# Kernel optimization log

Hardware: AMD Instinct MI355X
Metric: run time of the kernel (lower is better)

Reference implementation:

```python
import jax, jax.numpy as jnp
import numpy as np
import math

H = 256; LAT = 128; T = 1024; B = 64
FREQS = jnp.array([0.19, 0.21, 0.23, 0.25, 0.27, 0.29], dtype=jnp.float32)
EPS = 1e-5  # torch LayerNorm / BatchNorm default eps


def layer_norm(x, g, b):
    m = x.mean(-1, keepdims=True)
    v = jnp.var(x, axis=-1, keepdims=True)
    return (x - m) / jnp.sqrt(v + EPS) * g + b


def lrelu(x):
    return jax.nn.leaky_relu(x, 0.2)


def lstm_layer(x, wih, whh, bih, bhh):
    # x: [B,T,I] -> outputs [B,T,Hh]; PyTorch gate order i,f,g,o
    Hh = whh.shape[1]
    xg = jnp.einsum('bti,gi->btg', x, wih) + bih + bhh  # precomputed input contribution
    def step(carry, xg_t):
        h, c = carry
        gates = xg_t + h @ whh.T
        i, f, g, o = jnp.split(gates, 4, axis=-1)
        c = jax.nn.sigmoid(f) * c + jax.nn.sigmoid(i) * jnp.tanh(g)
        h = jax.nn.sigmoid(o) * jnp.tanh(c)
        return (h, c), h
    h0 = jnp.zeros((x.shape[0], Hh), x.dtype)
    _, hs = jax.lax.scan(step, (h0, h0), jnp.swapaxes(xg, 0, 1))
    return jnp.swapaxes(hs, 0, 1)


def conv1d(x, w, b, pad):
    # x [B,C,T], w [O,I,K]
    y = jax.lax.conv_general_dilated(x, w, (1,), [(pad, pad)],
                                     dimension_numbers=('NCH', 'OIH', 'NCH'))
    return y + b[None, :, None]


def bn_eval(x, g, b):
    # eval-mode BatchNorm1d with running_mean=0, running_var=1
    return x / jnp.sqrt(1.0 + EPS) * g[None, :, None] + b[None, :, None]


def setup_inputs() -> dict:
    key = jax.random.key(0)
    ks = iter(jax.random.split(key, 64))
    def w(shape, s=0.05):
        return (s * jax.random.normal(next(ks), shape)).astype(jnp.float32)
    z1 = jnp.zeros
    o1 = jnp.ones
    inp = dict(
        z=jax.random.normal(next(ks), (B, LAT), dtype=jnp.float32),
        labels=jax.random.randint(next(ks), (B,), 0, 4),
        emb=w((4, H)),
        np_w=w((H, LAT + H)), np_b=z1((H,)), np_ln_g=o1((H,)), np_ln_b=z1((H,)),
        c_wih=w((4 * H, 2 * H)), c_whh=w((4 * H, H)), c_bih=z1((4 * H,)), c_bhh=z1((4 * H,)),
        f0_wih=w((4 * H, 2 * H)), f0_whh=w((4 * H, H)), f0_bih=z1((4 * H,)), f0_bhh=z1((4 * H,)),
        f_wih=w((3, 4 * H, H)), f_whh=w((3, 4 * H, H)), f_bih=z1((3, 4 * H)), f_bhh=z1((3, 4 * H)),
        osc_w1=w((H, H)), osc_b1=z1((H,)), osc_ln_g=o1((H,)), osc_ln_b=z1((H,)),
        osc_w2=w((T, H)), osc_b2=z1((T,)),
        cp_w1=w((H // 2, 2 * H)), cp_b1=z1((H // 2,)), cp_ln_g=o1((H // 2,)), cp_ln_b=z1((H // 2,)),
        cp_w2=w((4, H // 2)), cp_b2=z1((4,)),
        sin_w=w((H // 2, 12)), sin_b=z1((H // 2,)),
        conv1_w=w((H, 2 * H, 5)), conv1_b=z1((H,)), bn1_g=o1((H,)), bn1_b=z1((H,)),
        conv2_w=w((H // 2, H, 3)), conv2_b=z1((H // 2,)), bn2_g=o1((H // 2,)), bn2_b=z1((H // 2,)),
        conv3_w=w((1, H // 2, 3)), conv3_b=z1((1,)),
        stress_w=jnp.full((1, 1, 1), 1.8, dtype=jnp.float32),
        amuse_w=jnp.array([[[0.15, 0.7, 0.15]]], dtype=jnp.float32),
        amuse_b=jnp.full((1,), -0.3, dtype=jnp.float32),
    )
    return inp


def reference(z, labels, emb, np_w, np_b, np_ln_g, np_ln_b,
              c_wih, c_whh, c_bih, c_bhh,
              f0_wih, f0_whh, f0_bih, f0_bhh,
              f_wih, f_whh, f_bih, f_bhh,
              osc_w1, osc_b1, osc_ln_g, osc_ln_b, osc_w2, osc_b2,
              cp_w1, cp_b1, cp_ln_g, cp_ln_b, cp_w2, cp_b2,
              sin_w, sin_b,
              conv1_w, conv1_b, bn1_g, bn1_b,
              conv2_w, conv2_b, bn2_g, bn2_b,
              conv3_w, conv3_b, stress_w, amuse_w, amuse_b):
    Bn = z.shape[0]
    le = emb[labels]                                                    # [B,H]
    h = lrelu(layer_norm(jnp.concatenate([z, le], -1) @ np_w.T + np_b, np_ln_g, np_ln_b))
    sig_in = jnp.concatenate([jnp.broadcast_to(h[:, None, :], (Bn, T, H)),
                              jnp.broadcast_to(le[:, None, :], (Bn, T, H))], -1)  # [B,T,2H]
    coarse = lstm_layer(sig_in, c_wih, c_whh, c_bih, c_bhh)
    fine = lstm_layer(sig_in, f0_wih, f0_whh, f0_bih, f0_bhh)
    for l in range(f_wih.shape[0]):
        fine = lstm_layer(fine, f_wih[l], f_whh[l], f_bih[l], f_bhh[l])
    osc = jnp.tanh(lrelu(layer_norm(h @ osc_w1.T + osc_b1, osc_ln_g, osc_ln_b)) @ osc_w2.T + osc_b2)[:, :, None]  # [B,T,1]
    t = jnp.linspace(0.0, 1.0, T)
    phases = 2.0 * math.pi * t[:, None] * FREQS[None, :] * T            # [T,6]
    sincos = jnp.concatenate([jnp.sin(phases), jnp.cos(phases)], -1)    # [T,12]
    sin_feat = sincos @ sin_w.T + sin_b                                 # [T,H/2]
    sin_mean = jnp.broadcast_to(sin_feat.mean(-1, keepdims=True)[None], (Bn, T, 1))
    feats = jnp.concatenate([coarse.mean(1), fine.mean(1)], -1)         # [B,2H] (vectorized per-sample loop)
    cp = jax.nn.sigmoid(lrelu(layer_norm(feats @ cp_w1.T + cp_b1, cp_ln_g, cp_ln_b)) @ cp_w2.T + cp_b2)  # [B,4]
    freq = 0.19 + 0.1 * cp[:, 0:1]
    amp = 1.0 + 2.0 * cp[:, 1:2]
    phase = 2.0 * math.pi * cp[:, 2:3]
    baseline = -0.5 + cp[:, 3:4]
    cardiac = (amp * jnp.sin(2.0 * math.pi * freq * T * t[None, :] + phase) + baseline)[:, :, None]  # [B,T,1]
    combined = jnp.swapaxes(jnp.concatenate([coarse, fine], -1), 1, 2)  # [B,2H,T]
    x = lrelu(bn_eval(conv1d(combined, conv1_w, conv1_b, 2), bn1_g, bn1_b))
    x = lrelu(bn_eval(conv1d(x, conv2_w, conv2_b, 1), bn2_g, bn2_b))
    base = jnp.swapaxes(jnp.tanh(conv1d(x, conv3_w, conv3_b, 1)), 1, 2)  # [B,T,1]
    enhanced = 0.1 * base + 0.1 * osc + 0.7 * cardiac + 0.1 * sin_mean
    # vectorized per-sample conditional routing (expert dispatch)
    et = jnp.swapaxes(enhanced, 1, 2)                                   # [B,1,T]
    stress = jnp.swapaxes(conv1d(et, stress_w, jnp.zeros((1,), et.dtype), 0), 1, 2)
    amuse = jnp.swapaxes(conv1d(et, amuse_w, amuse_b, 1), 1, 2)
    lab = labels[:, None, None]
    out = jnp.where(lab == 1, enhanced,
                    jnp.where(lab == 2, stress,
                              jnp.where(lab == 3, amuse, jnp.zeros_like(enhanced))))
    return out
```

## Files before the change

kernel.cpp:

```cpp
#include <hip/hip_runtime.h>

typedef _Float16 f16;
typedef _Float16 f16x2 __attribute__((ext_vector_type(2)));
typedef _Float16 f16x8 __attribute__((ext_vector_type(8)));
typedef float    f32x4 __attribute__((ext_vector_type(4)));

__device__ f16   g_Xpad [64u*1028u*512u];
__device__ f16   g_fseqA[64u*1024u*256u];
__device__ f16   g_fseqB[64u*1024u*256u];
__device__ f16   g_fseqC[64u*1024u*256u];
__device__ float g_xg32 [3u*64u*1048576u];
__device__ f16   g_c2in [64u*1026u*256u];
__device__ f16   g_c3in [64u*1024u*128u];
__device__ f16   g_whhT2[5u*262144u];
__device__ f16   g_wihO [3u*262144u];
__device__ float g_biasP[3*1024];
__device__ f16   g_B1   [256u*2560u];
__device__ f16   g_B2   [128u*768u];
__device__ float g_xg0  [2*64*1024];
__device__ float g_cat512[64*512];
__device__ float g_h    [64*256];
__device__ float g_feats[64*512];
__device__ float g_osc  [64*1024];
__device__ float g_smean[1024];
__device__ float g_cpar [64*4];
__device__ float g_enh  [64*1024];
__device__ unsigned g_hflag[3*64*128];
__device__ unsigned g_pflag[3*64*128];

__device__ inline float fdot2f(f16x2 a, f16x2 b, float c) {
#if __has_builtin(__builtin_amdgcn_fdot2)
  return __builtin_amdgcn_fdot2(a, b, c, false);
#else
  return c + (float)a[0]*(float)b[0] + (float)a[1]*(float)b[1];
#endif
}
__device__ inline float sigm_fast(float x) { return 1.0f / (1.0f + __expf(-x)); }
__device__ inline float tanh_fast(float x) { float e = __expf(2.0f*x); return 1.0f - 2.0f/(e + 1.0f); }
__device__ inline float lrelu(float x) { return x < 0.0f ? 0.2f*x : x; }
__device__ __forceinline__ void dot8x(f16x8 w, f16x8 h, float& a) {
  a = fdot2f(__builtin_shufflevector(w, w, 0, 1), __builtin_shufflevector(h, h, 0, 1), a);
  a = fdot2f(__builtin_shufflevector(w, w, 2, 3), __builtin_shufflevector(h, h, 2, 3), a);
  a = fdot2f(__builtin_shufflevector(w, w, 4, 5), __builtin_shufflevector(h, h, 4, 5), a);
  a = fdot2f(__builtin_shufflevector(w, w, 6, 7), __builtin_shufflevector(h, h, 6, 7), a);
}
__device__ __forceinline__ void wait_ge(const unsigned* p, unsigned want) {
  while (__hip_atomic_load(p, __ATOMIC_RELAXED, __HIP_MEMORY_SCOPE_AGENT) < want) {}
  unsigned v;
  do { v = __hip_atomic_load(p, __ATOMIC_ACQUIRE, __HIP_MEMORY_SCOPE_AGENT); } while (v < want);
}

__global__ void __launch_bounds__(256) k_prep_whh(const float* cw, const float* f0w, const float* fw) {
  int bid = blockIdx.x;
  int L = bid >> 10, g = bid & 1023, k = threadIdx.x;
  const float* src = (L == 0) ? cw : (L == 1) ? f0w : (fw + (size_t)(L-2)*262144u);
  int q = g >> 8, u = g & 255, r = u*4 + q;
  int ko = k >> 3, kl = k & 7;
  g_whhT2[(size_t)L*262144u + (size_t)(ko*1024 + r)*8u + kl] = (f16)src[(size_t)g*256 + k];
}
__global__ void __launch_bounds__(256) k_prep_wih(const float* fwih, const float* fbih, const float* fbhh) {
  int bid = blockIdx.x;
  int L = bid >> 10, g = bid & 1023, k = threadIdx.x;
  int q = g >> 8, u = g & 255, r = u*4 + q;
  int ko = k >> 3, kl = k & 7;
  g_wihO[(size_t)L*262144u + (size_t)(ko*1024 + r)*8u + kl] = (f16)fwih[(size_t)L*262144u + (size_t)g*256u + k];
  if (k == 0) g_biasP[L*1024 + r] = fbih[L*1024 + g] + fbhh[L*1024 + g];
}
__global__ void __launch_bounds__(256) k_prep_c1(const float* w) {
  int idx = blockIdx.x*256 + threadIdx.x;
  int oc = idx / 2560, rem = idx % 2560, r = rem / 512, ic = rem % 512;
  g_B1[idx] = (f16)w[(size_t)oc*2560 + (size_t)ic*5 + r];
}
__global__ void __launch_bounds__(256) k_prep_c2(const float* w) {
  int idx = blockIdx.x*256 + threadIdx.x;
  int oc = idx / 768, rem = idx % 768, r = rem / 256, ic = rem % 256;
  g_B2[idx] = (f16)w[(size_t)oc*768 + (size_t)ic*3 + r];
}
__global__ void __launch_bounds__(256) k_zero() {
  int idx = blockIdx.x*256 + threadIdx.x;
  if (idx < 131072) {
    int b = idx >> 11, rem = idx & 2047, rr = rem >> 9, c = rem & 511;
    int row = (rr < 2) ? rr : 1024 + rr;
    g_Xpad[(size_t)b*526336u + (size_t)row*512u + c] = (f16)0.0f;
  } else if (idx < 163840) {
    int i2 = idx - 131072;
    int b = i2 >> 9, rem = i2 & 511, rr = rem >> 8, c = rem & 255;
    int row = rr ? 1025 : 0;
    g_c2in[(size_t)b*262656u + (size_t)row*256u + c] = (f16)0.0f;
  } else {
    int i3 = idx - 163840;
    if (i3 < 24576) g_hflag[i3] = 0u;
    else            g_pflag[i3 - 24576] = 0u;
  }
}

__global__ void __launch_bounds__(256) k_setup1(const float* z, const int* labels, const float* emb,
                                                const float* npw, const float* npb,
                                                const float* lg, const float* lb) {
  __shared__ float x[384];
  __shared__ float s1[256], s2[256];
  int b = blockIdx.x, tid = threadIdx.x;
  int lab = labels[b];
  for (int i = tid; i < 384; i += 256)
    x[i] = (i < 128) ? z[b*128 + i] : emb[lab*256 + (i - 128)];
  __syncthreads();
  float acc = npb[tid];
  for (int k = 0; k < 384; ++k) acc += npw[tid*384 + k]*x[k];
  s1[tid] = acc; s2[tid] = acc*acc; __syncthreads();
  for (int s = 128; s > 0; s >>= 1) { if (tid < s) { s1[tid]+=s1[tid+s]; s2[tid]+=s2[tid+s]; } __syncthreads(); }
  float m = s1[0]*(1.0f/256.0f), var = s2[0]*(1.0f/256.0f) - m*m;
  float hv = (acc - m)*(1.0f/sqrtf(var + 1e-5f))*lg[tid] + lb[tid];
  hv = lrelu(hv);
  g_h[b*256 + tid] = hv;
  g_cat512[b*512 + tid] = hv;
  g_cat512[b*512 + 256 + tid] = x[128 + tid];
}
__global__ void __launch_bounds__(1024) k_xg0(const float* cwih, const float* cbih, const float* cbhh,
                                              const float* fwih, const float* fbih, const float* fbhh) {
  int bid = blockIdx.x;
  int layer = bid >> 6, b = bid & 63;
  int gp = threadIdx.x, j = gp >> 2, q = gp & 3, g = q*256 + j;
  __shared__ float cat[512];
  if (gp < 512) cat[gp] = g_cat512[b*512 + gp];
  __syncthreads();
  const float* w = layer ? fwih : cwih;
  float acc = layer ? (fbih[g] + fbhh[g]) : (cbih[g] + cbhh[g]);
  for (int k = 0; k < 512; ++k) acc += w[(size_t)g*512 + k]*cat[k];
  g_xg0[(layer*64 + b)*1024 + gp] = acc;
}
__global__ void __launch_bounds__(256) k_osc(const float* w1, const float* b1v, const float* lg,
                                             const float* lb, const float* w2, const float* b2v) {
  __shared__ float hb[256], av[256], s1[256], s2[256];
  int b = blockIdx.x, tid = threadIdx.x;
  hb[tid] = g_h[b*256 + tid];
  __syncthreads();
  float acc = b1v[tid];
  for (int k = 0; k < 256; ++k) acc += w1[tid*256 + k]*hb[k];
  s1[tid] = acc; s2[tid] = acc*acc; __syncthreads();
  for (int s = 128; s > 0; s >>= 1) { if (tid < s) { s1[tid]+=s1[tid+s]; s2[tid]+=s2[tid+s]; } __syncthreads(); }
  float m = s1[0]*(1.0f/256.0f), var = s2[0]*(1.0f/256.0f) - m*m;
  av[tid] = lrelu((acc - m)*(1.0f/sqrtf(var + 1e-5f))*lg[tid] + lb[tid]);
  __syncthreads();
  for (int tt = tid; tt < 1024; tt += 256) {
    float o = b2v[tt];
    for (int i = 0; i < 256; ++i) o += w2[(size_t)tt*256 + i]*av[i];
    g_osc[b*1024 + tt] = tanhf(o);
  }
}
__global__ void __launch_bounds__(256) k_sinmean(const float* sw, const float* sb) {
  int tt = blockIdx.x*256 + threadIdx.x;
  const float F[6] = {0.19f, 0.21f, 0.23f, 0.25f, 0.27f, 0.29f};
  float tl = tt*(1.0f/1023.0f);
  float sc[12];
  for (int j = 0; j < 6; ++j) {
    float p = (6.2831853071795864f * tl) * F[j] * 1024.0f;
    sc[j] = sinf(p); sc[6 + j] = cosf(p);
  }
  float a = 0.0f;
  for (int i = 0; i < 128; ++i) {
    float s = sb[i];
    for (int j = 0; j < 12; ++j) s += sw[i*12 + j]*sc[j];
    a += s;
  }
  g_smean[tt] = a*(1.0f/128.0f);
}

__global__ void __launch_bounds__(512, 2) k_chain() {
  int bid = blockIdx.x;
  int role = bid >> 6, b = bid & 63;
  int tau = threadIdx.x;
  bool isP = (role == 2) || (role == 4) || (role == 6);
  int lp = (role - 2) >> 1;
  int Lg = (role==0)?0:(role==1)?1:(role==3)?2:(role==5)?3:4;

  __shared__ __align__(16) f16 wlds[65536];
  __shared__ __align__(16) f16 hbuf[2][256];
  __shared__ __align__(16) float gbuf[1024];

  const f16* Wc = isP ? (g_wihO + (size_t)lp*262144u) : (g_whhT2 + (size_t)Lg*262144u);
#pragma unroll
  for (int i = 0; i < 16; ++i) {
    int o = i*512 + tau;
    *(f16x8*)(wlds + (size_t)o*8u) = *(const f16x8*)(Wc + (size_t)o*8u);
  }
  f16x8 wA[24], wB[24];
  {
    const f16* wp = Wc + (size_t)(8*1024 + tau)*8u;
#pragma unroll
    for (int i = 0; i < 24; ++i) {
      wA[i] = *(const f16x8*)(wp + (size_t)i*8192u);
      wB[i] = *(const f16x8*)(wp + (size_t)i*8192u + 4096u);
    }
  }

  if (isP) {
    const f16* hs = ((lp==0) ? g_fseqA : (lp==1) ? g_fseqB : g_fseqC) + (size_t)b*262144u;
    const unsigned* hf = g_hflag + (lp*64 + b)*128;
    float* xo = g_xg32 + (size_t)(lp*64 + b)*1048576u;
    unsigned* pf = g_pflag + (lp*64 + b)*128;
    float bA = g_biasP[lp*1024 + tau], bB = g_biasP[lp*1024 + 512 + tau];
    __syncthreads();
#pragma unroll 1
    for (int t = 0; t < 1024; ++t) {
      if ((t & 7) == 0) {
        if (tau == 0) wait_ge(hf + (t >> 3), (unsigned)(t >> 3) + 1u);
        __syncthreads();
      }
      if (tau < 32) *(f16x8*)(&hbuf[t & 1][tau*8]) = *(const f16x8*)(hs + (size_t)t*256u + tau*8);
      __syncthreads();
      const f16* hb = &hbuf[t & 1][0];
      float a0 = 0.f, a1 = 0.f, b0 = 0.f, b1 = 0.f;
#pragma unroll
      for (int ko = 0; ko < 8; ++ko) {
        f16x8 hv = *(const f16x8*)(hb + ko*8);
        f16x8 wa = *(const f16x8*)(wlds + (size_t)(ko*1024 + tau)*8u);
        f16x8 wb = *(const f16x8*)(wlds + (size_t)(ko*1024 + tau + 512)*8u);
        dot8x(wa, hv, a0); dot8x(wb, hv, b0);
      }
#pragma unroll
      for (int i = 0; i < 24; ++i) {
        f16x8 hv = *(const f16x8*)(hb + 64 + i*8);
        dot8x(wA[i], hv, a1); dot8x(wB[i], hv, b1);
      }
      xo[(size_t)t*1024u + tau]       = a0 + a1 + bA;
      xo[(size_t)t*1024u + 512 + tau] = b0 + b1 + bB;
      if ((t & 7) == 7) {
        __syncthreads();
        if (tau == 0) __hip_atomic_store(pf + (t >> 3), (unsigned)(t >> 3) + 1u,
                                         __ATOMIC_RELEASE, __HIP_MEMORY_SCOPE_AGENT);
      }
    }
  } else {
    bool dyn = (role >= 3);
    int lq = (role - 3) >> 1;
    float c0 = 0.0f, sum0 = 0.0f;
    f32x4 xg4 = {0.f, 0.f, 0.f, 0.f};
    const f32x4* xp = nullptr;
    const unsigned* xf = nullptr;
    f16* outp = nullptr; int ostride = 0;
    unsigned* hfo = nullptr;
    if (tau < 256) {
      hbuf[0][tau] = (f16)0.0f;
      if (!dyn) xg4 = *(const f32x4*)(g_xg0 + (size_t)(Lg*64 + b)*1024u + 4*tau);
      else      xp  = (const f32x4*)(g_xg32 + (size_t)(lq*64 + b)*1048576u) + tau;
      if (role == 0)      { outp = g_Xpad  + (size_t)b*526336u + 1024 + tau;       ostride = 512; }
      else if (role == 1) { outp = g_fseqA + (size_t)b*262144u + tau;              ostride = 256; }
      else if (role == 3) { outp = g_fseqB + (size_t)b*262144u + tau;              ostride = 256; }
      else if (role == 5) { outp = g_fseqC + (size_t)b*262144u + tau;              ostride = 256; }
      else                { outp = g_Xpad  + (size_t)b*526336u + 1024 + 256 + tau; ostride = 512; }
    }
    if (dyn) xf = g_pflag + (lq*64 + b)*128;
    int hop = (role == 1) ? 0 : (role == 3) ? 1 : (role == 5) ? 2 : -1;
    if (hop >= 0) hfo = g_hflag + (hop*64 + b)*128;
    __syncthreads();
    int cur = 0;
#pragma unroll 1
    for (int step = 0; step < 1024; ++step) {
      if (dyn && (step & 7) == 0) {
        if (tau == 0) wait_ge(xf + (step >> 3), (unsigned)(step >> 3) + 1u);
        __syncthreads();
      }
      f32x4 xv = xg4;
      if (dyn && tau < 256)
        xv = xp[(size_t)step*256u];
      const f16* hb = &hbuf[cur][0];
      float a0 = 0.f, a1 = 0.f, b0 = 0.f, b1 = 0.f;
#pragma unroll
      for (int ko = 0; ko < 8; ++ko) {
        f16x8 hv = *(const f16x8*)(hb + ko*8);
        f16x8 wa = *(const f16x8*)(wlds + (size_t)(ko*1024 + tau)*8u);
        f16x8 wb = *(const f16x8*)(wlds + (size_t)(ko*1024 + tau + 512)*8u);
        dot8x(wa, hv, a0); dot8x(wb, hv, b0);
      }
#pragma unroll
      for (int i = 0; i < 24; ++i) {
        f16x8 hv = *(const f16x8*)(hb + 64 + i*8);
        dot8x(wA[i], hv, a1); dot8x(wB[i], hv, b1);
      }
      gbuf[tau] = a0 + a1; gbuf[tau + 512] = b0 + b1;
      __syncthreads();
      if (tau < 256) {
        f32x4 gv = *(const f32x4*)(&gbuf[4*tau]);
        float ii = sigm_fast(gv[0] + xv[0]), ff = sigm_fast(gv[1] + xv[1]);
        float gg = tanh_fast(gv[2] + xv[2]), oo = sigm_fast(gv[3] + xv[3]);
        c0 = ff*c0 + ii*gg;
        float h0 = oo*tanh_fast(c0); sum0 += h0;
        hbuf[cur ^ 1][tau] = (f16)h0;
        outp[(size_t)step*ostride] = (f16)h0;
      }
      __syncthreads();
      if (hfo && (step & 7) == 7 && tau == 0)
        __hip_atomic_store(hfo + (step >> 3), (unsigned)(step >> 3) + 1u,
                           __ATOMIC_RELEASE, __HIP_MEMORY_SCOPE_AGENT);
      cur ^= 1;
    }
    if (tau < 256) {
      if (role == 0) g_feats[b*512 + tau]       = sum0*(1.0f/1024.0f);
      if (role == 7) g_feats[b*512 + 256 + tau] = sum0*(1.0f/1024.0f);
    }
  }
}

__global__ void __launch_bounds__(256) k_gemm(int which,
                                              const float* cb, const float* bng, const float* bnb) {
  const f16* A; size_t a_bs; int a_rs, K; const f16* Bm;
  f16* outH; size_t o_bs; int o_rs;
  if (which == 2) {
    A = g_Xpad; a_bs = 526336u; a_rs = 512; K = 2560; Bm = g_B1;
    outH = g_c2in + 256; o_bs = 262656u; o_rs = 256;
  } else {
    A = g_c2in; a_bs = 262656u; a_rs = 256; K = 768; Bm = g_B2;
    outH = g_c3in; o_bs = 131072u; o_rs = 128;
  }
  int tid = threadIdx.x, wave = tid >> 6, lane = tid & 63;
  int m0 = blockIdx.x*128, n0 = blockIdx.y*64;
  __shared__ __align__(16) f16 Asm[128*72];
  __shared__ __align__(16) f16 Bsm[64*72];
  f32x4 acc[2][4];
#pragma unroll
  for (int i = 0; i < 2; ++i)
#pragma unroll
    for (int jj = 0; jj < 4; ++jj) { f32x4 zz = {0.f,0.f,0.f,0.f}; acc[i][jj] = zz; }
  int ar = tid & 127, ac = (tid >> 7)*32;
  int mrow = m0 + ar, abb = mrow >> 10, att = mrow & 1023;
  const f16* aptr = A + (size_t)abb*a_bs + (size_t)att*a_rs + ac;
  int br = tid & 63, bc = (tid >> 6)*16;
  const f16* bptr = Bm + (size_t)(n0 + br)*K + bc;
  int nkb = K >> 6;
  for (int kb = 0; kb < nkb; ++kb) {
    f16x8 av0 = *(const f16x8*)(aptr + 0);
    f16x8 av1 = *(const f16x8*)(aptr + 8);
    f16x8 av2 = *(const f16x8*)(aptr + 16);
    f16x8 av3 = *(const f16x8*)(aptr + 24);
    f16x8 bv0 = *(const f16x8*)(bptr + 0);
    f16x8 bv1 = *(const f16x8*)(bptr + 8);
    aptr += 64; bptr += 64;
    __syncthreads();
    *(f16x8*)(&Asm[ar*72 + ac + 0])  = av0;
    *(f16x8*)(&Asm[ar*72 + ac + 8])  = av1;
    *(f16x8*)(&Asm[ar*72 + ac + 16]) = av2;
    *(f16x8*)(&Asm[ar*72 + ac + 24]) = av3;
    *(f16x8*)(&Bsm[br*72 + bc + 0])  = bv0;
    *(f16x8*)(&Bsm[br*72 + bc + 8])  = bv1;
    __syncthreads();
#pragma unroll
    for (int ks = 0; ks < 2; ++ks) {
      int ko = ks*32 + (lane >> 4)*8;
      f16x8 a0 = *(const f16x8*)(&Asm[(wave*32 + (lane & 15))*72 + ko]);
      f16x8 a1 = *(const f16x8*)(&Asm[(wave*32 + 16 + (lane & 15))*72 + ko]);
#pragma unroll
      for (int nt = 0; nt < 4; ++nt) {
        f16x8 bf = *(const f16x8*)(&Bsm[(nt*16 + (lane & 15))*72 + ko]);
        acc[0][nt] = __builtin_amdgcn_mfma_f32_16x16x32_f16(a0, bf, acc[0][nt], 0, 0, 0);
        acc[1][nt] = __builtin_amdgcn_mfma_f32_16x16x32_f16(a1, bf, acc[1][nt], 0, 0, 0);
      }
    }
  }
  const float bnc = 0.99999500003749969f;
#pragma unroll
  for (int mt = 0; mt < 2; ++mt)
#pragma unroll
    for (int nt = 0; nt < 4; ++nt)
#pragma unroll
      for (int r = 0; r < 4; ++r) {
        int m_loc = wave*32 + mt*16 + (lane >> 4)*4 + r;
        int n = n0 + nt*16 + (lane & 15);
        int mg = m0 + m_loc, ob = mg >> 10, ot = mg & 1023;
        float v = acc[mt][nt][r];
        v = (v + cb[n])*(bng[n]*bnc) + bnb[n];
        v = lrelu(v);
        outH[(size_t)ob*o_bs + (size_t)ot*o_rs + n] = (f16)v;
      }
}

__global__ void __launch_bounds__(128) k_cp(const float* w1, const float* b1v, const float* lg,
                                            const float* lb, const float* w2, const float* b2v) {
  __shared__ float ft[512], av[128], s1[128], s2[128];
  int b = blockIdx.x, tid = threadIdx.x;
  for (int i = tid; i < 512; i += 128) ft[i] = g_feats[b*512 + i];
  __syncthreads();
  float acc = b1v[tid];
  for (int k = 0; k < 512; ++k) acc += w1[tid*512 + k]*ft[k];
  s1[tid] = acc; s2[tid] = acc*acc; __syncthreads();
  for (int s = 64; s > 0; s >>= 1) { if (tid < s) { s1[tid]+=s1[tid+s]; s2[tid]+=s2[tid+s]; } __syncthreads(); }
  float m = s1[0]*(1.0f/128.0f), var = s2[0]*(1.0f/128.0f) - m*m;
  av[tid] = lrelu((acc - m)*(1.0f/sqrtf(var + 1e-5f))*lg[tid] + lb[tid]);
  __syncthreads();
  if (tid < 4) {
    float s = b2v[tid];
    for (int i = 0; i < 128; ++i) s += w2[tid*128 + i]*av[i];
    g_cpar[b*4 + tid] = 1.0f/(1.0f + expf(-s));
  }
}

__global__ void __launch_bounds__(256) k_enh(const float* w3, const float* b3) {
  int idx = blockIdx.x*256 + threadIdx.x;
  int b = idx >> 10, t = idx & 1023;
  const f16* xc = g_c3in + (size_t)idx*128u;
  bool hm = (t > 0), hp = (t < 1023);
  float pre = b3[0];
  for (int c = 0; c < 128; ++c) {
    float xm = hm ? (float)xc[c - 128] : 0.0f;
    float x0 = (float)xc[c];
    float xp = hp ? (float)xc[c + 128] : 0.0f;
    pre += xm*w3[c*3] + x0*w3[c*3 + 1] + xp*w3[c*3 + 2];
  }
  float base = tanhf(pre);
  float cp0 = g_cpar[b*4 + 0], cp1 = g_cpar[b*4 + 1], cp2 = g_cpar[b*4 + 2], cp3 = g_cpar[b*4 + 3];
  float freq  = 0.19f + 0.1f*cp0;
  float amp   = 1.0f + 2.0f*cp1;
  float phase = 6.2831853071795864f*cp2;
  float basel = -0.5f + cp3;
  float tl = t*(1.0f/1023.0f);
  float arg = ((6.2831853071795864f*freq)*1024.0f)*tl + phase;
  float card = amp*sinf(arg) + basel;
  g_enh[idx] = 0.1f*base + 0.1f*g_osc[idx] + 0.7f*card + 0.1f*g_smean[t];
}

__global__ void __launch_bounds__(256) k_out(const int* labels, const float* sw,
                                             const float* aw, const float* ab, float* out) {
  int idx = blockIdx.x*256 + threadIdx.x;
  int b = idx >> 10, t = idx & 1023;
  int lab = labels[b];
  float e = g_enh[idx], r;
  if (lab == 1) r = e;
  else if (lab == 2) r = sw[0]*e;
  else if (lab == 3) {
    float em = (t > 0)    ? g_enh[idx - 1] : 0.0f;
    float ep = (t < 1023) ? g_enh[idx + 1] : 0.0f;
    r = aw[0]*em + aw[1]*e + aw[2]*ep + ab[0];
  } else r = 0.0f;
  out[idx] = r;
}

extern "C" void kernel_launch(void* const* d_in, const int* in_sizes, int n_in,
                              void* d_out, int out_size, void* d_ws, size_t ws_size,
                              hipStream_t stream) {
  const float* z       = (const float*)d_in[0];
  const int*   labels  = (const int*)  d_in[1];
  const float* emb     = (const float*)d_in[2];
  const float* np_w    = (const float*)d_in[3];
  const float* np_b    = (const float*)d_in[4];
  const float* np_ln_g = (const float*)d_in[5];
  const float* np_ln_b = (const float*)d_in[6];
  const float* c_wih   = (const float*)d_in[7];
  const float* c_whh   = (const float*)d_in[8];
  const float* c_bih   = (const float*)d_in[9];
  const float* c_bhh   = (const float*)d_in[10];
  const float* f0_wih  = (const float*)d_in[11];
  const float* f0_whh  = (const float*)d_in[12];
  const float* f0_bih  = (const float*)d_in[13];
  const float* f0_bhh  = (const float*)d_in[14];
  const float* f_wih   = (const float*)d_in[15];
  const float* f_whh   = (const float*)d_in[16];
  const float* f_bih   = (const float*)d_in[17];
  const float* f_bhh   = (const float*)d_in[18];
  const float* osc_w1  = (const float*)d_in[19];
  const float* osc_b1  = (const float*)d_in[20];
  const float* osc_ln_g= (const float*)d_in[21];
  const float* osc_ln_b= (const float*)d_in[22];
  const float* osc_w2  = (const float*)d_in[23];
  const float* osc_b2  = (const float*)d_in[24];
  const float* cp_w1   = (const float*)d_in[25];
  const float* cp_b1   = (const float*)d_in[26];
  const float* cp_ln_g = (const float*)d_in[27];
  const float* cp_ln_b = (const float*)d_in[28];
  const float* cp_w2   = (const float*)d_in[29];
  const float* cp_b2   = (const float*)d_in[30];
  const float* sin_w   = (const float*)d_in[31];
  const float* sin_b   = (const float*)d_in[32];
  const float* conv1_w = (const float*)d_in[33];
  const float* conv1_b = (const float*)d_in[34];
  const float* bn1_g   = (const float*)d_in[35];
  const float* bn1_b   = (const float*)d_in[36];
  const float* conv2_w = (const float*)d_in[37];
  const float* conv2_b = (const float*)d_in[38];
  const float* bn2_g   = (const float*)d_in[39];
  const float* bn2_b   = (const float*)d_in[40];
  const float* conv3_w = (const float*)d_in[41];
  const float* conv3_b = (const float*)d_in[42];
  const float* stress_w= (const float*)d_in[43];
  const float* amuse_w = (const float*)d_in[44];
  const float* amuse_b = (const float*)d_in[45];
  float* out = (float*)d_out;

  k_prep_whh<<<5120, 256, 0, stream>>>(c_whh, f0_whh, f_whh);
  k_prep_wih<<<3072, 256, 0, stream>>>(f_wih, f_bih, f_bhh);
  k_prep_c1 <<<2560, 256, 0, stream>>>(conv1_w);
  k_prep_c2 <<< 384, 256, 0, stream>>>(conv2_w);
  k_zero    <<< 832, 256, 0, stream>>>();
  k_setup1  <<<  64, 256, 0, stream>>>(z, labels, emb, np_w, np_b, np_ln_g, np_ln_b);
  k_xg0     <<< 128,1024, 0, stream>>>(c_wih, c_bih, c_bhh, f0_wih, f0_bih, f0_bhh);
  k_osc     <<<  64, 256, 0, stream>>>(osc_w1, osc_b1, osc_ln_g, osc_ln_b, osc_w2, osc_b2);
  k_sinmean <<<   4, 256, 0, stream>>>(sin_w, sin_b);

  k_chain   <<< 512, 512, 0, stream>>>();

  k_cp      <<<  64, 128, 0, stream>>>(cp_w1, cp_b1, cp_ln_g, cp_ln_b, cp_w2, cp_b2);
  k_gemm    <<<dim3(512, 4), 256, 0, stream>>>(2, conv1_b, bn1_g, bn1_b);
  k_gemm    <<<dim3(512, 2), 256, 0, stream>>>(3, conv2_b, bn2_g, bn2_b);
  k_enh     <<< 256, 256, 0, stream>>>(conv3_w, conv3_b);
  k_out     <<< 256, 256, 0, stream>>>(labels, stress_w, amuse_w, amuse_b, out);
}
```

Before: 4.866 ms.

## Split LSTM recurrent matvec over K halves with four gate rows per thread

Each thread previously computed two full-K dot products over 256 inputs. It now computes four output rows over one half of K (kh = tau>>8), and the two halves are reduced through a doubled gbuf in shared memory. Each h vector load is reused across four weight rows, and the LDS and register weight layouts are permuted to match. This adds an extra shared-memory reduction stage and changes which weights sit in registers versus LDS. The goal is to cut the shared-memory reads of h per step and raise instruction-level parallelism in the serial recurrence.

```diff
diff --git a/kernel.cpp b/kernel.cpp
--- a/kernel.cpp
+++ b/kernel.cpp
@@ -169,36 +169,37 @@
   int bid = blockIdx.x;
   int role = bid >> 6, b = bid & 63;
   int tau = threadIdx.x;
+  int kh = tau >> 8, j = tau & 255;
   bool isP = (role == 2) || (role == 4) || (role == 6);
   int lp = (role - 2) >> 1;
   int Lg = (role==0)?0:(role==1)?1:(role==3)?2:(role==5)?3:4;
 
   __shared__ __align__(16) f16 wlds[65536];
   __shared__ __align__(16) f16 hbuf[2][256];
-  __shared__ __align__(16) float gbuf[1024];
+  __shared__ __align__(16) float gbuf[2048];
 
   const f16* Wc = isP ? (g_wihO + (size_t)lp*262144u) : (g_whhT2 + (size_t)Lg*262144u);
 #pragma unroll
   for (int i = 0; i < 16; ++i) {
     int o = i*512 + tau;
-    *(f16x8*)(wlds + (size_t)o*8u) = *(const f16x8*)(Wc + (size_t)o*8u);
-  }
-  f16x8 wA[24], wB[24];
-  {
-    const f16* wp = Wc + (size_t)(8*1024 + tau)*8u;
-#pragma unroll
-    for (int i = 0; i < 24; ++i) {
-      wA[i] = *(const f16x8*)(wp + (size_t)i*8192u);
-      wB[i] = *(const f16x8*)(wp + (size_t)i*8192u + 4096u);
-    }
-  }
+    int p = o >> 10, rr = o & 1023;
+    int ko = (p < 4) ? p : (p + 12);
+    *(f16x8*)(wlds + (size_t)o*8u) = *(const f16x8*)(Wc + (size_t)(ko*1024 + rr)*8u);
+  }
+  f16x8 wR[48];
+#pragma unroll
+  for (int m = 0; m < 12; ++m)
+#pragma unroll
+    for (int i = 0; i < 4; ++i)
+      wR[m*4 + i] = *(const f16x8*)(Wc + (size_t)((16*kh + 4 + m)*1024 + j + 256*i)*8u);
 
   if (isP) {
     const f16* hs = ((lp==0) ? g_fseqA : (lp==1) ? g_fseqB : g_fseqC) + (size_t)b*262144u;
     const unsigned* hf = g_hflag + (lp*64 + b)*128;
     float* xo = g_xg32 + (size_t)(lp*64 + b)*1048576u;
     unsigned* pf = g_pflag + (lp*64 + b)*128;
-    float bA = g_biasP[lp*1024 + tau], bB = g_biasP[lp*1024 + 512 + tau];
+    f32x4 bias4 = {0.f,0.f,0.f,0.f};
+    if (tau < 256) bias4 = *(const f32x4*)(g_biasP + lp*1024 + 4*tau);
     __syncthreads();
 #pragma unroll 1
     for (int t = 0; t < 1024; ++t) {
@@ -208,22 +209,38 @@
       }
       if (tau < 32) *(f16x8*)(&hbuf[t & 1][tau*8]) = *(const f16x8*)(hs + (size_t)t*256u + tau*8);
       __syncthreads();
-      const f16* hb = &hbuf[t & 1][0];
-      float a0 = 0.f, a1 = 0.f, b0 = 0.f, b1 = 0.f;
-#pragma unroll
-      for (int ko = 0; ko < 8; ++ko) {
-        f16x8 hv = *(const f16x8*)(hb + ko*8);
-        f16x8 wa = *(const f16x8*)(wlds + (size_t)(ko*1024 + tau)*8u);
-        f16x8 wb = *(const f16x8*)(wlds + (size_t)(ko*1024 + tau + 512)*8u);
-        dot8x(wa, hv, a0); dot8x(wb, hv, b0);
-      }
-#pragma unroll
-      for (int i = 0; i < 24; ++i) {
-        f16x8 hv = *(const f16x8*)(hb + 64 + i*8);
-        dot8x(wA[i], hv, a1); dot8x(wB[i], hv, b1);
-      }
-      xo[(size_t)t*1024u + tau]       = a0 + a1 + bA;
-      xo[(size_t)t*1024u + 512 + tau] = b0 + b1 + bB;
+      const f16* hb = &hbuf[t & 1][kh*128];
+      float p0 = 0.f, p1 = 0.f, p2 = 0.f, p3 = 0.f;
+#pragma unroll
+      for (int c = 0; c < 4; ++c) {
+        f16x8 hv = *(const f16x8*)(hb + c*8);
+        int pl = 4*kh + c;
+        dot8x(*(const f16x8*)(wlds + (size_t)(pl*1024 + j)*8u),       hv, p0);
+        dot8x(*(const f16x8*)(wlds + (size_t)(pl*1024 + j + 256)*8u), hv, p1);
+        dot8x(*(const f16x8*)(wlds + (size_t)(pl*1024 + j + 512)*8u), hv, p2);
+        dot8x(*(const f16x8*)(wlds + (size_t)(pl*1024 + j + 768)*8u), hv, p3);
+      }
+#pragma unroll
+      for (int m = 0; m < 12; ++m) {
+        f16x8 hv = *(const f16x8*)(hb + 32 + m*8);
+        dot8x(wR[m*4 + 0], hv, p0);
+        dot8x(wR[m*4 + 1], hv, p1);
+        dot8x(wR[m*4 + 2], hv, p2);
+        dot8x(wR[m*4 + 3], hv, p3);
+      }
+      gbuf[kh*1024 + j]       = p0;
+      gbuf[kh*1024 + j + 256] = p1;
+      gbuf[kh*1024 + j + 512] = p2;
+      gbuf[kh*1024 + j + 768] = p3;
+      __syncthreads();
+      if (tau < 256) {
+        f32x4 gA = *(const f32x4*)(&gbuf[4*tau]);
+        f32x4 gB = *(const f32x4*)(&gbuf[1024 + 4*tau]);
+        f32x4 v;
+        v[0] = gA[0] + gB[0] + bias4[0]; v[1] = gA[1] + gB[1] + bias4[1];
+        v[2] = gA[2] + gB[2] + bias4[2]; v[3] = gA[3] + gB[3] + bias4[3];
+        *(f32x4*)(xo + (size_t)t*1024u + 4*tau) = v;
+      }
       if ((t & 7) == 7) {
         __syncthreads();
         if (tau == 0) __hip_atomic_store(pf + (t >> 3), (unsigned)(t >> 3) + 1u,
@@ -263,26 +280,37 @@
       f32x4 xv = xg4;
       if (dyn && tau < 256)
         xv = xp[(size_t)step*256u];
-      const f16* hb = &hbuf[cur][0];
-      float a0 = 0.f, a1 = 0.f, b0 = 0.f, b1 = 0.f;
-#pragma unroll
-      for (int ko = 0; ko < 8; ++ko) {
-        f16x8 hv = *(const f16x8*)(hb + ko*8);
-        f16x8 wa = *(const f16x8*)(wlds + (size_t)(ko*1024 + tau)*8u);
-        f16x8 wb = *(const f16x8*)(wlds + (size_t)(ko*1024 + tau + 512)*8u);
-        dot8x(wa, hv, a0); dot8x(wb, hv, b0);
-      }
-#pragma unroll
-      for (int i = 0; i < 24; ++i) {
-        f16x8 hv = *(const f16x8*)(hb + 64 + i*8);
-        dot8x(wA[i], hv, a1); dot8x(wB[i], hv, b1);
-      }
-      gbuf[tau] = a0 + a1; gbuf[tau + 512] = b0 + b1;
+      const f16* hb = &hbuf[cur][kh*128];
+      float p0 = 0.f, p1 = 0.f, p2 = 0.f, p3 = 0.f;
+#pragma unroll
+      for (int c = 0; c < 4; ++c) {
+        f16x8 hv = *(const f16x8*)(hb + c*8);
+        int pl = 4*kh + c;
+        dot8x(*(const f16x8*)(wlds + (size_t)(pl*1024 + j)*8u),       hv, p0);
+        dot8x(*(const f16x8*)(wlds + (size_t)(pl*1024 + j + 256)*8u), hv, p1);
+        dot8x(*(const f16x8*)(wlds + (size_t)(pl*1024 + j + 512)*8u), hv, p2);
+        dot8x(*(const f16x8*)(wlds + (size_t)(pl*1024 + j + 768)*8u), hv, p3);
+      }
+#pragma unroll
+      for (int m = 0; m < 12; ++m) {
+        f16x8 hv = *(const f16x8*)(hb + 32 + m*8);
+        dot8x(wR[m*4 + 0], hv, p0);
+        dot8x(wR[m*4 + 1], hv, p1);
+        dot8x(wR[m*4 + 2], hv, p2);
+        dot8x(wR[m*4 + 3], hv, p3);
+      }
+      gbuf[kh*1024 + j]       = p0;
+      gbuf[kh*1024 + j + 256] = p1;
+      gbuf[kh*1024 + j + 512] = p2;
+      gbuf[kh*1024 + j + 768] = p3;
       __syncthreads();
       if (tau < 256) {
-        f32x4 gv = *(const f32x4*)(&gbuf[4*tau]);
-        float ii = sigm_fast(gv[0] + xv[0]), ff = sigm_fast(gv[1] + xv[1]);
-        float gg = tanh_fast(gv[2] + xv[2]), oo = sigm_fast(gv[3] + xv[3]);
+        f32x4 gA = *(const f32x4*)(&gbuf[4*tau]);
+        f32x4 gB = *(const f32x4*)(&gbuf[1024 + 4*tau]);
+        float ii = sigm_fast(gA[0] + gB[0] + xv[0]);
+        float ff = sigm_fast(gA[1] + gB[1] + xv[1]);
+        float gg = tanh_fast(gA[2] + gB[2] + xv[2]);
+        float oo = sigm_fast(gA[3] + gB[3] + xv[3]);
         c0 = ff*c0 + ii*gg;
         float h0 = oo*tanh_fast(c0); sum0 += h0;
         hbuf[cur ^ 1][tau] = (f16)h0;
```

After: 4.822 ms (median of 2 runs). Within noise of the previous version (-0.9%).
